# Optimization experiments

Hardware: AMD Instinct MI355X
Metric: run time of the kernel (lower is better)

## Reference

```python
import jax, jax.numpy as jnp
import numpy as np
from jax.scipy.special import logsumexp

B, F, V, C, K, KP = 8192, 32, 64, 32, 8, 7  # batch, features, values/feature, classes, gate options, padded pair candidates
TEMP = 1.0
EPS = 1e-06


def _structure():
    # candidate 0 = self table; candidates 1..7 = pair tables conditioned on preceding features
    mask = np.zeros((F - 1, K), dtype=bool)
    mask[:, 0] = True
    cond = np.zeros((F - 1, KP), dtype=np.int32)
    for i in range(F - 1):
        fi = i + 1
        for j in range(min(fi, KP)):
            mask[i, j + 1] = True
            cond[i, j] = fi - 1 - j
    return jnp.asarray(cond), jnp.asarray(mask)


def setup_inputs() -> dict:
    key = jax.random.key(0)
    ks = jax.random.split(key, 6)
    cond_index, valid_mask = _structure()
    return {
        "x": jax.random.randint(ks[0], (B, F), 0, V, dtype=jnp.int32),
        "training": True,
        "class_logits": jax.random.normal(ks[1], (C,), jnp.float32) * 0.1,
        "table0": jax.random.normal(ks[2], (V, C), jnp.float32) * 0.1,
        "self_tables": jax.random.normal(ks[3], (F - 1, V, C), jnp.float32) * 0.1,
        "pair_tables": jax.random.normal(ks[4], (F - 1, KP, V, V, C), jnp.float32) * 0.1,
        "structure_logits": jax.random.normal(ks[5], (F - 1, K), jnp.float32) * 0.1,
        "u_noise": jax.random.uniform(jax.random.fold_in(key, 7), (F - 1, K), jnp.float32),
        "cond_index": cond_index,
        "valid_mask": valid_mask,
    }


def reference(x, training, class_logits, table0, self_tables, pair_tables,
              structure_logits, u_noise, cond_index, valid_mask):
    # class prior term
    cl = class_logits - logsumexp(class_logits)  # [C]
    t0 = table0 - logsumexp(table0, axis=0, keepdims=True)  # [V,C]
    out = cl[None, :] + t0[x[:, 0]]  # [B,C]

    # Gumbel-softmax gate over candidate parent sets (training path)
    g = -jnp.log(-jnp.log(u_noise + EPS) + EPS)
    gate_logits = jnp.where(valid_mask, (structure_logits + g) / TEMP, -jnp.inf)
    w = jax.nn.softmax(gate_logits, axis=-1)  # [F-1,K]; padded entries get weight 0

    f_idx = jnp.arange(F - 1)
    xs = x[:, 1:]  # [B,F-1] feature values

    # self (class-only) candidate tables, normalized over the feature-value axis
    st = self_tables - logsumexp(self_tables, axis=1, keepdims=True)  # [F-1,V,C]
    self_g = st[f_idx[None, :], xs]  # [B,F-1,C]
    out = out + jnp.einsum('bfc,f->bc', self_g, w[:, 0])

    # pair candidate tables, normalized over the feature-value axis (axis 2)
    pt = pair_tables - logsumexp(pair_tables, axis=2, keepdims=True)  # [F-1,KP,V,V,C]
    xc = x[:, cond_index]  # [B,F-1,KP] conditioning feature values
    k_idx = jnp.arange(KP)
    pair_g = pt[f_idx[None, :, None], k_idx[None, None, :], xs[:, :, None], xc]  # [B,F-1,KP,C]
    out = out + jnp.einsum('bfkc,fk->bc', pair_g, w[:, 1:])
    return out
```

## Files before the change

### kernel.cpp

```cpp
#include <hip/hip_runtime.h>
#include <math.h>

#define B_  8192
#define F_  32
#define V_  64
#define C_  32
#define KP_ 7
#define EPS_ 1e-6f

typedef float f4 __attribute__((ext_vector_type(4)));

#define WS_OFF  256
#define WS_G    512
#define WS_LSE  66048
#define LSE_BANK4 111104
#define WS_PART 1843712

#define NBLK_LSE 868
#define NBLK_PAIR 2048

__device__ const int d_split[9] = {0, 25, 50, 74, 99, 123, 148, 172, 196};

__global__ __launch_bounds__(256)
void fused_kernel(const int* __restrict__ x, const float* __restrict__ pt,
                  const float* __restrict__ cl, const float* __restrict__ t0,
                  const float* __restrict__ st, const float* __restrict__ sl,
                  const float* __restrict__ un, float* __restrict__ ws) {
    if (blockIdx.x < NBLK_LSE) {
        int fk = blockIdx.x >> 2;
        int qa = blockIdx.x & 3;
        int t  = threadIdx.x;
        const f4* __restrict__ p =
            (const f4*)(pt + (size_t)fk * (V_ * V_ * C_)
                           + (size_t)qa * 16 * (V_ * C_));
        const f4* p0 = p + t;
        const f4* p1 = p + 256 + t;
        f4 s0 = (f4)(0.f);
        f4 s1 = (f4)(0.f);
        #pragma unroll 4
        for (int a = 0; a < 16; a++) {
            f4 l0 = __builtin_nontemporal_load(p0 + a * 512);
            f4 l1 = __builtin_nontemporal_load(p1 + a * 512);
            s0.x += __expf(l0.x); s0.y += __expf(l0.y);
            s0.z += __expf(l0.z); s0.w += __expf(l0.w);
            s1.x += __expf(l1.x); s1.y += __expf(l1.y);
            s1.z += __expf(l1.z); s1.w += __expf(l1.w);
        }
        f4* lseP = (f4*)(ws + WS_LSE) + (size_t)qa * LSE_BANK4;
        __builtin_nontemporal_store(s0, lseP + fk * 512 + t);
        __builtin_nontemporal_store(s1, lseP + fk * 512 + 256 + t);
    } else if (blockIdx.x == NBLK_LSE) {
        __shared__ float gl[31][8];
        __shared__ float wsm[31][8];
        __shared__ float lsf[31][32];
        int tid = threadIdx.x;
        if (tid < 248) {
            int f = tid >> 3, k = tid & 7;
            int kmax = min(f + 1, KP_);
            bool valid = (k <= kmax);
            float u = un[tid];
            float g = -__logf(-__logf(u + EPS_) + EPS_);
            gl[f][k] = valid ? (sl[tid] + g) : -INFINITY;
        } else {
            ws[tid] = 0.f;
        }
        __syncthreads();
        if (tid < 248) {
            int f = tid >> 3, k = tid & 7;
            float m = -INFINITY;
            #pragma unroll
            for (int j = 0; j < 8; j++) m = fmaxf(m, gl[f][j]);
            float s = 0.f;
            #pragma unroll
            for (int j = 0; j < 8; j++) s += __expf(gl[f][j] - m);
            float wv = __expf(gl[f][k] - m) / s;
            wsm[f][k] = wv;
            ws[tid] = wv;
        }
        for (int i = tid; i < 992; i += 256) {
            int f = i >> 5, c = i & 31;
            float s = 0.f;
            #pragma unroll 8
            for (int v = 0; v < V_; v++) s += __expf(st[(f * V_ + v) * C_ + c]);
            lsf[f][c] = __logf(s);
        }
        __syncthreads();
        if (tid < 32) {
            int c = tid;
            float scl = 0.f;
            #pragma unroll
            for (int j = 0; j < C_; j++) scl += __expf(cl[j]);
            float lse_cl = __logf(scl);
            float s0 = 0.f;
            #pragma unroll 8
            for (int v = 0; v < V_; v++) s0 += __expf(t0[v * C_ + c]);
            float lse_t0 = __logf(s0);
            float acc = cl[c] - lse_cl - lse_t0;
            for (int f = 0; f < 31; f++) acc -= wsm[f][0] * lsf[f][c];
            ws[WS_OFF + c] = acc;
        }
    } else {
        __shared__ int   xsh[32][33];
        __shared__ float wsh[256];
        __shared__ int   etab[200];
        __shared__ float gl[31][8];
        int tid = threadIdx.x;
        int pb    = blockIdx.x - (NBLK_LSE + 1);
        int g     = pb & 7;
        int chunk = pb >> 3;
        int s0    = chunk * 32;
        for (int i = tid; i < 1024; i += 256)
            xsh[i >> 5][i & 31] = x[s0 * 32 + i];
        if (tid < 248) {
            int f = tid >> 3, k = tid & 7;
            int kmax = min(f + 1, KP_);
            bool valid = (k <= kmax);
            float u = un[tid];
            float gg = -__logf(-__logf(u + EPS_) + EPS_);
            gl[f][k] = valid ? (sl[tid] + gg) : -INFINITY;
        }
        if (tid < 200) {
            int q = tid / 25, i = tid % 25;
            int e = d_split[q] + i;
            int packed;
            if (e < d_split[q + 1]) {
                int f = 0, base = 0;
                for (;;) { int cnt = min(f + 1, KP_); if (e < base + cnt) break; base += cnt; f++; }
                int k = e - base;
                packed = ((f * 8 + k + 1) << 20) | ((f * KP_ + k) << 12) | ((f + 1) << 6) | (f - k);
            } else {
                packed = (248 << 20);
            }
            etab[tid] = packed;
        }
        __syncthreads();
        if (tid < 248) {
            int f = tid >> 3;
            float m = -INFINITY;
            #pragma unroll
            for (int j = 0; j < 8; j++) m = fmaxf(m, gl[f][j]);
            float s = 0.f;
            #pragma unroll
            for (int j = 0; j < 8; j++) s += __expf(gl[f][j] - m);
            wsh[tid] = __expf(gl[f][tid & 7] - m) / s;
        } else {
            wsh[tid] = 0.f;
        }
        __syncthreads();

        int s  = tid >> 3;
        int c4 = tid & 7;
        const int* xrow = xsh[s];
        const float* __restrict__ ptb = pt + c4 * 4;
        float4 acc = make_float4(0.f, 0.f, 0.f, 0.f);

        int beg = g * 25;
        #pragma unroll
        for (int ch = 0; ch < 5; ch++) {
            float4 pv[5];
            float  wt[5];
            #pragma unroll
            for (int i = 0; i < 5; i++) {
                int pk = etab[beg + ch * 5 + i];
                int ci = pk & 63, fi = (pk >> 6) & 63;
                int fk = (pk >> 12) & 255, widx = (pk >> 20) & 255;
                int xv = xrow[fi], xc = xrow[ci];
                pv[i] = *(const float4*)(ptb + ((size_t)(fk * V_ + xv) * V_ + xc) * C_);
                wt[i] = wsh[widx];
            }
            #pragma unroll
            for (int i = 0; i < 5; i++) {
                acc.x += wt[i] * pv[i].x; acc.y += wt[i] * pv[i].y;
                acc.z += wt[i] * pv[i].z; acc.w += wt[i] * pv[i].w;
            }
        }
        ((float4*)(ws + WS_PART))[(size_t)(s0 + s) * 64 + g * 8 + c4] = acc;
    }
}

__global__ __launch_bounds__(256)
void foldg_kernel(const float* __restrict__ t0, const float* __restrict__ st,
                  float* __restrict__ ws) {
    int idx = blockIdx.x * 256 + threadIdx.x;
    int c4 = idx & 7, v = (idx >> 3) & 63, j = idx >> 9;
    int nk = min(KP_, 31 - j);
    const float4* lse4 = (const float4*)(ws + WS_LSE);
    float4 g;
    if (j == 0) {
        g = ((const float4*)t0)[v * 8 + c4];
    } else {
        float w0 = ws[(j - 1) * 8];
        float4 sv = ((const float4*)st)[((j - 1) * V_ + v) * 8 + c4];
        g.x = w0 * sv.x; g.y = w0 * sv.y; g.z = w0 * sv.z; g.w = w0 * sv.w;
    }
    for (int k = 0; k < nk; k++) {
        int f = j + k;
        float wv = ws[f * 8 + k + 1];
        int iq = ((f * KP_ + k) * V_ + v) * 8 + c4;
        float4 sa = lse4[iq];
        float4 sb = lse4[1 * LSE_BANK4 + iq];
        float4 sc = lse4[2 * LSE_BANK4 + iq];
        float4 sd = lse4[3 * LSE_BANK4 + iq];
        g.x -= wv * __logf(sa.x + sb.x + sc.x + sd.x);
        g.y -= wv * __logf(sa.y + sb.y + sc.y + sd.y);
        g.z -= wv * __logf(sa.z + sb.z + sc.z + sd.z);
        g.w -= wv * __logf(sa.w + sb.w + sc.w + sd.w);
    }
    ((float4*)(ws + WS_G))[idx] = g;
}

__global__ __launch_bounds__(256)
void maing_kernel(const int* __restrict__ x, const float* __restrict__ ws,
                  float* __restrict__ out) {
    __shared__ int    xsh[32][33];
    __shared__ float4 offv[8];
    int tid = threadIdx.x;
    int rbase = blockIdx.x * 32;
    for (int i = tid; i < 1024; i += 256) {
        int rr = i >> 5, jj = i & 31;
        xsh[rr][jj] = x[(rbase + rr) * 32 + jj];
    }
    if (tid < 8) offv[tid] = ((const float4*)(ws + WS_OFF))[tid];
    __syncthreads();
    int r = tid >> 3, c4 = tid & 7;
    const float4* __restrict__ G4 = (const float4*)(ws + WS_G);
    float4 acc = offv[c4];
    const float4* __restrict__ pp =
        (const float4*)(ws + WS_PART) + (size_t)(rbase + r) * 64 + c4;
    #pragma unroll
    for (int g = 0; g < 8; g++) {
        float4 t = pp[g * 8];
        acc.x += t.x; acc.y += t.y; acc.z += t.z; acc.w += t.w;
    }
    #pragma unroll 8
    for (int j = 0; j < 32; j++) {
        float4 gv = G4[(j * V_ + xsh[r][j]) * 8 + c4];
        acc.x += gv.x; acc.y += gv.y; acc.z += gv.z; acc.w += gv.w;
    }
    ((float4*)out)[(rbase + r) * 8 + c4] = acc;
}

extern "C" void kernel_launch(void* const* d_in, const int* in_sizes, int n_in,
                              void* d_out, int out_size, void* d_ws, size_t ws_size,
                              hipStream_t stream) {
    const int*   x   = (const int*)  d_in[0];
    const float* cl  = (const float*)d_in[2];
    const float* t0  = (const float*)d_in[3];
    const float* st  = (const float*)d_in[4];
    const float* pt  = (const float*)d_in[5];
    const float* sl  = (const float*)d_in[6];
    const float* un  = (const float*)d_in[7];
    float* ws  = (float*)d_ws;
    float* out = (float*)d_out;

    fused_kernel<<<NBLK_LSE + 1 + NBLK_PAIR, 256, 0, stream>>>(x, pt, cl, t0, st, sl, un, ws);
    foldg_kernel<<<64, 256, 0, stream>>>(t0, st, ws);
    maing_kernel<<<256, 256, 0, stream>>>(x, ws, out);
}
```

Before: 221.3 us.

## Write fp16 copy of pair tables during LSE pass and gather from it when ready

```diff
diff --git a/kernel.cpp b/kernel.cpp
--- a/kernel.cpp
+++ b/kernel.cpp
@@ -1,4 +1,5 @@
 #include <hip/hip_runtime.h>
+#include <hip/hip_fp16.h>
 #include <math.h>
 
 #define B_  8192
@@ -9,18 +10,24 @@
 #define EPS_ 1e-6f
 
 typedef float f4 __attribute__((ext_vector_type(4)));
+typedef unsigned int u2 __attribute__((ext_vector_type(2)));
 
 #define WS_OFF  256
 #define WS_G    512
 #define WS_LSE  66048
 #define LSE_BANK4 111104
 #define WS_PART 1843712
+#define WS_CTR  4000000
+#define WS_H    4194304ull
+#define H_BYTES (217ull * V_ * V_ * C_ * 2ull)
+#define NEED_WS (WS_H * 4ull + H_BYTES)
 
 #define NBLK_LSE 868
 #define NBLK_PAIR 2048
 
 __device__ const int d_split[9] = {0, 25, 50, 74, 99, 123, 148, 172, 196};
 
+template<int CVT>
 __global__ __launch_bounds__(256)
 void fused_kernel(const int* __restrict__ x, const float* __restrict__ pt,
                   const float* __restrict__ cl, const float* __restrict__ t0,
@@ -35,12 +42,29 @@
                            + (size_t)qa * 16 * (V_ * C_));
         const f4* p0 = p + t;
         const f4* p1 = p + 256 + t;
+        __half* shw = (__half*)(ws + WS_H) + (size_t)fk * (V_ * V_ * C_)
+                                           + (size_t)qa * 16 * (V_ * C_);
         f4 s0 = (f4)(0.f);
         f4 s1 = (f4)(0.f);
         #pragma unroll 4
         for (int a = 0; a < 16; a++) {
             f4 l0 = __builtin_nontemporal_load(p0 + a * 512);
             f4 l1 = __builtin_nontemporal_load(p1 + a * 512);
+            if (CVT) {
+                __half2 h0a = __floats2half2_rn(l0.x, l0.y);
+                __half2 h0b = __floats2half2_rn(l0.z, l0.w);
+                __half2 h1a = __floats2half2_rn(l1.x, l1.y);
+                __half2 h1b = __floats2half2_rn(l1.z, l1.w);
+                unsigned w0a = *(unsigned*)&h0a;
+                unsigned w0b = *(unsigned*)&h0b;
+                unsigned w1a = *(unsigned*)&h1a;
+                unsigned w1b = *(unsigned*)&h1b;
+                u2 v0, v1;
+                v0.x = w0a; v0.y = w0b;
+                v1.x = w1a; v1.y = w1b;
+                __builtin_nontemporal_store(v0, (u2*)(shw + (size_t)a * 2048 + 4 * t));
+                __builtin_nontemporal_store(v1, (u2*)(shw + (size_t)a * 2048 + 1024 + 4 * t));
+            }
             s0.x += __expf(l0.x); s0.y += __expf(l0.y);
             s0.z += __expf(l0.z); s0.w += __expf(l0.w);
             s1.x += __expf(l1.x); s1.y += __expf(l1.y);
@@ -49,6 +73,15 @@
         f4* lseP = (f4*)(ws + WS_LSE) + (size_t)qa * LSE_BANK4;
         __builtin_nontemporal_store(s0, lseP + fk * 512 + t);
         __builtin_nontemporal_store(s1, lseP + fk * 512 + 256 + t);
+        if (CVT) {
+            __threadfence();
+            __syncthreads();
+            if (t == 0) {
+                int* done = (int*)ws + WS_CTR;
+                __hip_atomic_fetch_add(&done[fk], 1, __ATOMIC_RELEASE,
+                                       __HIP_MEMORY_SCOPE_AGENT);
+            }
+        }
     } else if (blockIdx.x == NBLK_LSE) {
         __shared__ float gl[31][8];
         __shared__ float wsm[31][8];
@@ -134,6 +167,14 @@
             etab[tid] = packed;
         }
         __syncthreads();
+        if (CVT && tid < 25) {
+            int slot = g * 25 + tid;
+            int fkE = (etab[slot] >> 12) & 255;
+            int* done = (int*)ws + WS_CTR;
+            int v = __hip_atomic_load(&done[fkE], __ATOMIC_ACQUIRE,
+                                      __HIP_MEMORY_SCOPE_AGENT);
+            if (v == 4) etab[slot] |= (1 << 30);
+        }
         if (tid < 248) {
             int f = tid >> 3;
             float m = -INFINITY;
@@ -151,7 +192,8 @@
         int s  = tid >> 3;
         int c4 = tid & 7;
         const int* xrow = xsh[s];
-        const float* __restrict__ ptb = pt + c4 * 4;
+        const float*  __restrict__ ptb = pt + c4 * 4;
+        const __half* __restrict__ shh = (const __half*)(ws + WS_H);
         float4 acc = make_float4(0.f, 0.f, 0.f, 0.f);
 
         int beg = g * 25;
@@ -165,7 +207,19 @@
                 int ci = pk & 63, fi = (pk >> 6) & 63;
                 int fk = (pk >> 12) & 255, widx = (pk >> 20) & 255;
                 int xv = xrow[fi], xc = xrow[ci];
-                pv[i] = *(const float4*)(ptb + ((size_t)(fk * V_ + xv) * V_ + xc) * C_);
+                size_t eoff = ((size_t)(fk * V_ + xv) * V_ + xc) * C_;
+                if (CVT && (pk & (1 << 30))) {
+                    u2 hv = *(const u2*)(shh + eoff + c4 * 4);
+                    unsigned ua = hv.x;
+                    unsigned ub = hv.y;
+                    __half2 ha = *(__half2*)&ua;
+                    __half2 hb = *(__half2*)&ub;
+                    float2 f0 = __half22float2(ha);
+                    float2 f1 = __half22float2(hb);
+                    pv[i] = make_float4(f0.x, f0.y, f1.x, f1.y);
+                } else {
+                    pv[i] = *(const float4*)(ptb + eoff);
+                }
                 wt[i] = wsh[widx];
             }
             #pragma unroll
@@ -253,7 +307,12 @@
     float* ws  = (float*)d_ws;
     float* out = (float*)d_out;
 
-    fused_kernel<<<NBLK_LSE + 1 + NBLK_PAIR, 256, 0, stream>>>(x, pt, cl, t0, st, sl, un, ws);
+    if (ws_size >= NEED_WS) {
+        (void)hipMemsetAsync(ws + WS_CTR, 0, 217 * sizeof(int), stream);
+        fused_kernel<1><<<NBLK_LSE + 1 + NBLK_PAIR, 256, 0, stream>>>(x, pt, cl, t0, st, sl, un, ws);
+    } else {
+        fused_kernel<0><<<NBLK_LSE + 1 + NBLK_PAIR, 256, 0, stream>>>(x, pt, cl, t0, st, sl, un, ws);
+    }
     foldg_kernel<<<64, 256, 0, stream>>>(t0, st, ws);
     maing_kernel<<<256, 256, 0, stream>>>(x, ws, out);
 }
```

Measured after the change: 457.2 us. +106.6%, slower.
